# Performance work log

Hardware: AMD Instinct MI355X
Metric: run time of the kernel (lower is better)

The kernel has to match this reference:

```python
import jax, jax.numpy as jnp
import numpy as np

N_HEAD, D_MODEL, D_VOCAB = 8, 512, 32000
B, P = 8, 512


def setup_inputs() -> dict:
    key = jax.random.key(0)
    k_x, k_w, k_b = jax.random.split(key, 3)
    input_tensor = jax.random.normal(k_x, (B, P, N_HEAD, D_MODEL), dtype=jnp.float32)
    # per-head Linear params, torch layout: weight [d_vocab, d_model], bias [d_vocab]
    bound = 1.0 / np.sqrt(D_MODEL)
    weights = jax.random.uniform(k_w, (N_HEAD, D_VOCAB, D_MODEL), minval=-bound, maxval=bound, dtype=jnp.float32)
    biases = jax.random.uniform(k_b, (N_HEAD, D_VOCAB), minval=-bound, maxval=bound, dtype=jnp.float32)
    return {"input_tensor": input_tensor, "weights": weights, "biases": biases}


def reference(input_tensor, weights, biases) -> jnp.ndarray:
    # sum_h (x[:,:,h,:] @ W_h^T + b_h)  -> single contraction over (h, d)
    # input_tensor: [B, P, H, D]; weights: [H, V, D]; biases: [H, V]
    out = jnp.einsum("bphd,hvd->bpv", input_tensor, weights)
    out = out + biases.sum(axis=0)  # [V] broadcast over [B, P, V]
    return out
```

## Files before the change

### kernel.cpp

```cpp
#include <hip/hip_runtime.h>
#include <hip/hip_bf16.h>
#include <stdint.h>

#define NHEAD 8
#define DMODEL 512
#define DVOCAB 32000
#define M_DIM 4096
#define K_DIM 4096
#define N_DIM 32000
#define NT    64

typedef short bf16x8 __attribute__((ext_vector_type(8)));
typedef float f32x4 __attribute__((ext_vector_type(4)));
typedef unsigned short ushort8 __attribute__((ext_vector_type(8)));

template <int V> struct IC { static constexpr int v = V; };

__device__ __forceinline__ unsigned short f2bf(float f) {
    unsigned int u = __builtin_bit_cast(unsigned int, f);
    u = (u + 0x7fffu + ((u >> 16) & 1u)) >> 16;
    return (unsigned short)u;
}

__device__ __forceinline__ void load16_to_lds(const void* g, void* l) {
    __builtin_amdgcn_global_load_lds(
        (const __attribute__((address_space(1))) unsigned int*)g,
        (__attribute__((address_space(3))) unsigned int*)l, 16, 0, 0);
}

__global__ void cvt_x(const float* __restrict__ in, unsigned short* __restrict__ out) {
    long t = (long)blockIdx.x * 256 + threadIdx.x;
    const float4* s = (const float4*)in + t * 2;
    float4 a = s[0], b = s[1];
    ushort8 o;
    o[0] = f2bf(a.x); o[1] = f2bf(a.y); o[2] = f2bf(a.z); o[3] = f2bf(a.w);
    o[4] = f2bf(b.x); o[5] = f2bf(b.y); o[6] = f2bf(b.z); o[7] = f2bf(b.w);
    *(ushort8*)(out + t * 8) = o;
}

__global__ void cvt_w(const float* __restrict__ in, unsigned short* __restrict__ out) {
    int t = blockIdx.x * 256 + threadIdx.x;
    int d8 = t & 63;
    int hv = t >> 6;
    int h = hv / DVOCAB;
    int v = hv - h * DVOCAB;
    const float4* s = (const float4*)(in + (long)hv * DMODEL + d8 * 8);
    float4 a = s[0], b = s[1];
    ushort8 o;
    o[0] = f2bf(a.x); o[1] = f2bf(a.y); o[2] = f2bf(a.z); o[3] = f2bf(a.w);
    o[4] = f2bf(b.x); o[5] = f2bf(b.y); o[6] = f2bf(b.z); o[7] = f2bf(b.w);
    *(ushort8*)(out + (long)v * K_DIM + h * DMODEL + d8 * 8) = o;
}

__global__ void bias_red(const float* __restrict__ b, float* __restrict__ out) {
    int v = blockIdx.x * 256 + threadIdx.x;
    if (v >= DVOCAB) return;
    float s = 0.f;
    #pragma unroll
    for (int h = 0; h < NHEAD; ++h) s += b[h * DVOCAB + v];
    out[v] = s;
}

#define BAR()    __builtin_amdgcn_s_barrier()
#define LGKM0()  asm volatile("s_waitcnt lgkmcnt(0)" ::: "memory")
#define VMCNT6() asm volatile("s_waitcnt vmcnt(6)" ::: "memory")
#define VMCNT0() asm volatile("s_waitcnt vmcnt(0)" ::: "memory")

__global__ __launch_bounds__(512, 2) void gemm256(
    const unsigned short* __restrict__ A,
    const unsigned short* __restrict__ B,
    const float* __restrict__ bias,
    float* __restrict__ C)
{
    __shared__ __attribute__((aligned(16))) unsigned short lds[2][2][2][8192];

    const int tid = threadIdx.x;
    const int bid = blockIdx.x;
    const int wg = (bid & 7) * 250 + (bid >> 3);
    const int mt = wg & 15;
    const int nt = wg >> 4;
    const long m0 = (long)mt * 256;
    const long n0 = (long)nt * 256;

    const int wid = tid >> 6, lane = tid & 63;
    const int wr = wid >> 2, wc = wid & 3;
    const int lr = lane & 15, lk = lane >> 4;
    const int swz = lr & 7;

    const unsigned short* pA[2];
    const unsigned short* pB[2];
    #pragma unroll
    for (int ks = 0; ks < 2; ++ks) {
        const int ch = ((ks << 2) | lk) ^ swz;
        pA[ks] = &lds[0][0][0][0] + (wr * 64 + lr) * 64 + ch * 8;
        pB[ks] = &lds[1][0][0][0] + (wc * 32 + lr) * 64 + ch * 8;
    }
    #define LDA(mi, ks, HALF, CURB) \
        (*(const bf16x8*)(pA[ks] + (mi) * 1024 + (HALF) * 16384 + (CURB) * 8192))
    #define LDB(nj, ks, HALF, CURB) \
        (*(const bf16x8*)(pB[ks] + (nj) * 1024 + (HALF) * 16384 + (CURB) * 8192))

    const char* Ab = (const char*)(A + m0 * K_DIM);
    const char* Bb = (const char*)(B + n0 * K_DIM);
    const int row0 = tid >> 3,         c0 = (tid & 7) ^ (row0 & 7);
    const int row1 = (512 + tid) >> 3, c1 = ((512 + tid) & 7) ^ (row1 & 7);
    unsigned int a00 = (unsigned)(row0 * K_DIM + c0 * 8) * 2u;
    unsigned int a01 = (unsigned)(row1 * K_DIM + c1 * 8) * 2u;
    unsigned int a10 = (unsigned)((128 + row0) * K_DIM + c0 * 8) * 2u;
    unsigned int a11 = (unsigned)((128 + row1) * K_DIM + c1 * 8) * 2u;
    unsigned int b00 = a00, b01 = a01, b10 = a10, b11 = a11;

    #define ST_A0(CURB) do { \
        load16_to_lds(Ab + a00, (char*)&lds[0][0][(CURB)][0] + tid * 16); \
        load16_to_lds(Ab + a01, (char*)&lds[0][0][(CURB)][0] + 8192 + tid * 16); \
        a00 += 128; a01 += 128; } while (0)
    #define ST_A1(CURB) do { \
        load16_to_lds(Ab + a10, (char*)&lds[0][1][(CURB)][0] + tid * 16); \
        load16_to_lds(Ab + a11, (char*)&lds[0][1][(CURB)][0] + 8192 + tid * 16); \
        a10 += 128; a11 += 128; } while (0)
    #define ST_B0(CURB) do { \
        load16_to_lds(Bb + b00, (char*)&lds[1][0][(CURB)][0] + tid * 16); \
        load16_to_lds(Bb + b01, (char*)&lds[1][0][(CURB)][0] + 8192 + tid * 16); \
        b00 += 128; b01 += 128; } while (0)
    #define ST_B1(CURB) do { \
        load16_to_lds(Bb + b10, (char*)&lds[1][1][(CURB)][0] + tid * 16); \
        load16_to_lds(Bb + b11, (char*)&lds[1][1][(CURB)][0] + 8192 + tid * 16); \
        b10 += 128; b11 += 128; } while (0)

    f32x4 acc[8][4];
    #pragma unroll
    for (int i = 0; i < 8; ++i)
        #pragma unroll
        for (int j = 0; j < 4; ++j)
            acc[i][j] = (f32x4){0.f, 0.f, 0.f, 0.f};

    bf16x8 af[4][2], bf0[2][2], bf1[2][2];

    ST_A0(0); ST_B0(0); ST_B1(0); ST_A1(0);
    ST_A0(1); ST_B0(1); ST_B1(1);
    VMCNT6();
    BAR();

    auto body = [&](auto curc, int t) {
        constexpr int CUR = decltype(curc)::v;

        #pragma unroll
        for (int mi = 0; mi < 4; ++mi) {
            af[mi][0] = LDA(mi, 0, 0, CUR);
            af[mi][1] = LDA(mi, 1, 0, CUR);
        }
        #pragma unroll
        for (int nj = 0; nj < 2; ++nj) {
            bf0[nj][0] = LDB(nj, 0, 0, CUR);
            bf0[nj][1] = LDB(nj, 1, 0, CUR);
        }
        if (t + 1 < NT) ST_A1(CUR ^ 1);
        BAR(); LGKM0();
        __builtin_amdgcn_s_setprio(1);
        #pragma unroll
        for (int mi = 0; mi < 4; ++mi)
            #pragma unroll
            for (int nj = 0; nj < 2; ++nj)
                #pragma unroll
                for (int ks = 0; ks < 2; ++ks)
                    acc[mi][nj] = __builtin_amdgcn_mfma_f32_16x16x32_bf16(
                        af[mi][ks], bf0[nj][ks], acc[mi][nj], 0, 0, 0);
        __builtin_amdgcn_s_setprio(0);
        BAR();

        #pragma unroll
        for (int nj = 0; nj < 2; ++nj) {
            bf1[nj][0] = LDB(nj, 0, 1, CUR);
            bf1[nj][1] = LDB(nj, 1, 1, CUR);
        }
        if (t + 2 < NT) ST_A0(CUR);
        BAR(); LGKM0();
        __builtin_amdgcn_s_setprio(1);
        #pragma unroll
        for (int mi = 0; mi < 4; ++mi)
            #pragma unroll
            for (int nj = 0; nj < 2; ++nj)
                #pragma unroll
                for (int ks = 0; ks < 2; ++ks)
                    acc[mi][2 + nj] = __builtin_amdgcn_mfma_f32_16x16x32_bf16(
                        af[mi][ks], bf1[nj][ks], acc[mi][2 + nj], 0, 0, 0);
        __builtin_amdgcn_s_setprio(0);
        BAR();

        #pragma unroll
        for (int mi = 0; mi < 4; ++mi) {
            af[mi][0] = LDA(mi, 0, 1, CUR);
            af[mi][1] = LDA(mi, 1, 1, CUR);
        }
        if (t + 2 < NT) ST_B0(CUR);
        BAR(); LGKM0();
        __builtin_amdgcn_s_setprio(1);
        #pragma unroll
        for (int mi = 0; mi < 4; ++mi)
            #pragma unroll
            for (int nj = 0; nj < 2; ++nj)
                #pragma unroll
                for (int ks = 0; ks < 2; ++ks)
                    acc[4 + mi][nj] = __builtin_amdgcn_mfma_f32_16x16x32_bf16(
                        af[mi][ks], bf0[nj][ks], acc[4 + mi][nj], 0, 0, 0);
        __builtin_amdgcn_s_setprio(0);
        BAR();

        if (t + 2 < NT) ST_B1(CUR);
        if (t < NT - 2) { VMCNT6(); } else { VMCNT0(); }
        BAR();
        __builtin_amdgcn_s_setprio(1);
        #pragma unroll
        for (int mi = 0; mi < 4; ++mi)
            #pragma unroll
            for (int nj = 0; nj < 2; ++nj)
                #pragma unroll
                for (int ks = 0; ks < 2; ++ks)
                    acc[4 + mi][2 + nj] = __builtin_amdgcn_mfma_f32_16x16x32_bf16(
                        af[mi][ks], bf1[nj][ks], acc[4 + mi][2 + nj], 0, 0, 0);
        __builtin_amdgcn_s_setprio(0);
        BAR();
    };

    for (int t = 0; t < NT; t += 2) {
        body(IC<0>{}, t);
        body(IC<1>{}, t + 1);
    }
    #undef LDA
    #undef LDB
    #undef ST_A0
    #undef ST_A1
    #undef ST_B0
    #undef ST_B1

    #pragma unroll
    for (int nj = 0; nj < 4; ++nj) {
        const long col = n0 + (nj >> 1) * 128 + wc * 32 + (nj & 1) * 16 + lr;
        const float bs = bias[col];
        #pragma unroll
        for (int mi = 0; mi < 8; ++mi) {
            const long row = m0 + (mi >> 2) * 128 + wr * 64 + (mi & 3) * 16 + lk * 4;
            #pragma unroll
            for (int r = 0; r < 4; ++r)
                __builtin_nontemporal_store(acc[mi][nj][r] + bs,
                                            &C[(row + r) * (long)N_DIM + col]);
        }
    }
}

__global__ void naive_out(const float* __restrict__ x, const float* __restrict__ w,
                          const float* __restrict__ b, float* __restrict__ out) {
    long idx = (long)blockIdx.x * 256 + threadIdx.x;
    if (idx >= (long)M_DIM * N_DIM) return;
    long m = idx / N_DIM;
    int v = (int)(idx - m * N_DIM);
    float s = 0.f;
    for (int h = 0; h < NHEAD; ++h) {
        const float* xr = x + m * K_DIM + h * DMODEL;
        const float* wr = w + ((long)h * DVOCAB + v) * DMODEL;
        float ps = 0.f;
        for (int d = 0; d < DMODEL; ++d) ps += xr[d] * wr[d];
        s += ps + b[h * DVOCAB + v];
    }
    out[idx] = s;
}

extern "C" void kernel_launch(void* const* d_in, const int* in_sizes, int n_in,
                              void* d_out, int out_size, void* d_ws, size_t ws_size,
                              hipStream_t stream) {
    const float* x = (const float*)d_in[0];
    const float* w = (const float*)d_in[1];
    const float* b = (const float*)d_in[2];
    float* out = (float*)d_out;

    const size_t xbf_bytes = (size_t)M_DIM * K_DIM * 2;
    const size_t wbf_bytes = (size_t)N_DIM * K_DIM * 2;
    const size_t bs_bytes  = (size_t)N_DIM * 4;
    const size_t need = xbf_bytes + wbf_bytes + bs_bytes;

    if (ws_size < need) {
        long total = (long)M_DIM * N_DIM;
        int blocks = (int)((total + 255) / 256);
        naive_out<<<blocks, 256, 0, stream>>>(x, w, b, out);
        return;
    }

    unsigned short* xbf = (unsigned short*)d_ws;
    unsigned short* wbf = (unsigned short*)((char*)d_ws + xbf_bytes);
    float* bsum = (float*)((char*)d_ws + xbf_bytes + wbf_bytes);

    cvt_x<<<8192, 256, 0, stream>>>(x, xbf);
    cvt_w<<<64000, 256, 0, stream>>>(w, wbf);
    bias_red<<<125, 256, 0, stream>>>(b, bsum);
    gemm256<<<2000, 512, 0, stream>>>(xbf, wbf, bsum, out);
}
```

Measured before the change: 1.085 ms.

## Software-pipeline LDS fragment reads across iterations and drop explicit lgkmcnt waits

Restructures the GEMM main loop so LDS fragment reads for the next tile are issued before the last MFMA quadrant of the current tile. A-fragments are double-buffered in registers (afL/afH), and explicit lgkmcnt(0) waits plus one barrier per phase are removed. Global-to-LDS prefetches are regrouped so the full second stage is in flight before the loop starts. The aim is to hide LDS latency behind MFMA work and cut barrier stalls, at the cost of more registers and tighter ordering assumptions on LDS hazards.

```diff
diff --git a/kernel.cpp b/kernel.cpp
--- a/kernel.cpp
+++ b/kernel.cpp
@@ -62,7 +62,7 @@
 }
 
 #define BAR()    __builtin_amdgcn_s_barrier()
-#define LGKM0()  asm volatile("s_waitcnt lgkmcnt(0)" ::: "memory")
+#define VMCNT8() asm volatile("s_waitcnt vmcnt(8)" ::: "memory")
 #define VMCNT6() asm volatile("s_waitcnt vmcnt(6)" ::: "memory")
 #define VMCNT0() asm volatile("s_waitcnt vmcnt(0)" ::: "memory")
 
@@ -127,6 +127,19 @@
         load16_to_lds(Bb + b11, (char*)&lds[1][1][(CURB)][0] + 8192 + tid * 16); \
         b10 += 128; b11 += 128; } while (0)
 
+    #define MFQUAD(AF, BF, MO, NO) do {                                        \
+        _Pragma("unroll")                                                      \
+        for (int ks = 0; ks < 2; ++ks)                                         \
+            _Pragma("unroll")                                                  \
+            for (int mi = 0; mi < 4; ++mi)                                     \
+                _Pragma("unroll")                                              \
+                for (int nj = 0; nj < 2; ++nj)                                 \
+                    acc[(MO) + mi][(NO) + nj] =                                \
+                        __builtin_amdgcn_mfma_f32_16x16x32_bf16(               \
+                            AF[mi][ks], BF[nj][ks], acc[(MO) + mi][(NO) + nj], \
+                            0, 0, 0);                                          \
+    } while (0)
+
     f32x4 acc[8][4];
     #pragma unroll
     for (int i = 0; i < 8; ++i)
@@ -134,92 +147,70 @@
         for (int j = 0; j < 4; ++j)
             acc[i][j] = (f32x4){0.f, 0.f, 0.f, 0.f};
 
-    bf16x8 af[4][2], bf0[2][2], bf1[2][2];
+    bf16x8 afL[4][2], afH[4][2], bf0[2][2], bf1[2][2];
 
     ST_A0(0); ST_B0(0); ST_B1(0); ST_A1(0);
-    ST_A0(1); ST_B0(1); ST_B1(1);
-    VMCNT6();
+    ST_A0(1); ST_B0(1); ST_B1(1); ST_A1(1);
+    VMCNT8();
     BAR();
+    #pragma unroll
+    for (int mi = 0; mi < 4; ++mi) {
+        afL[mi][0] = LDA(mi, 0, 0, 0);
+        afL[mi][1] = LDA(mi, 1, 0, 0);
+    }
+    #pragma unroll
+    for (int nj = 0; nj < 2; ++nj) {
+        bf0[nj][0] = LDB(nj, 0, 0, 0);
+        bf0[nj][1] = LDB(nj, 1, 0, 0);
+    }
 
     auto body = [&](auto curc, int t) {
         constexpr int CUR = decltype(curc)::v;
-
-        #pragma unroll
-        for (int mi = 0; mi < 4; ++mi) {
-            af[mi][0] = LDA(mi, 0, 0, CUR);
-            af[mi][1] = LDA(mi, 1, 0, CUR);
-        }
-        #pragma unroll
-        for (int nj = 0; nj < 2; ++nj) {
-            bf0[nj][0] = LDB(nj, 0, 0, CUR);
-            bf0[nj][1] = LDB(nj, 1, 0, CUR);
-        }
-        if (t + 1 < NT) ST_A1(CUR ^ 1);
-        BAR(); LGKM0();
-        __builtin_amdgcn_s_setprio(1);
-        #pragma unroll
-        for (int mi = 0; mi < 4; ++mi)
-            #pragma unroll
-            for (int nj = 0; nj < 2; ++nj)
-                #pragma unroll
-                for (int ks = 0; ks < 2; ++ks)
-                    acc[mi][nj] = __builtin_amdgcn_mfma_f32_16x16x32_bf16(
-                        af[mi][ks], bf0[nj][ks], acc[mi][nj], 0, 0, 0);
-        __builtin_amdgcn_s_setprio(0);
-        BAR();
 
         #pragma unroll
         for (int nj = 0; nj < 2; ++nj) {
             bf1[nj][0] = LDB(nj, 0, 1, CUR);
             bf1[nj][1] = LDB(nj, 1, 1, CUR);
         }
-        if (t + 2 < NT) ST_A0(CUR);
-        BAR(); LGKM0();
-        __builtin_amdgcn_s_setprio(1);
-        #pragma unroll
-        for (int mi = 0; mi < 4; ++mi)
-            #pragma unroll
-            for (int nj = 0; nj < 2; ++nj)
-                #pragma unroll
-                for (int ks = 0; ks < 2; ++ks)
-                    acc[mi][2 + nj] = __builtin_amdgcn_mfma_f32_16x16x32_bf16(
-                        af[mi][ks], bf1[nj][ks], acc[mi][2 + nj], 0, 0, 0);
+        __builtin_amdgcn_s_setprio(1);
+        MFQUAD(afL, bf0, 0, 0);
         __builtin_amdgcn_s_setprio(0);
         BAR();
 
+        if (t + 2 < NT) { ST_A0(CUR); ST_B0(CUR); }
         #pragma unroll
         for (int mi = 0; mi < 4; ++mi) {
-            af[mi][0] = LDA(mi, 0, 1, CUR);
-            af[mi][1] = LDA(mi, 1, 1, CUR);
-        }
-        if (t + 2 < NT) ST_B0(CUR);
-        BAR(); LGKM0();
-        __builtin_amdgcn_s_setprio(1);
-        #pragma unroll
-        for (int mi = 0; mi < 4; ++mi)
-            #pragma unroll
-            for (int nj = 0; nj < 2; ++nj)
-                #pragma unroll
-                for (int ks = 0; ks < 2; ++ks)
-                    acc[4 + mi][nj] = __builtin_amdgcn_mfma_f32_16x16x32_bf16(
-                        af[mi][ks], bf0[nj][ks], acc[4 + mi][nj], 0, 0, 0);
+            afH[mi][0] = LDA(mi, 0, 1, CUR);
+            afH[mi][1] = LDA(mi, 1, 1, CUR);
+        }
+        __builtin_amdgcn_s_setprio(1);
+        MFQUAD(afL, bf1, 0, 2);
         __builtin_amdgcn_s_setprio(0);
         BAR();
 
         if (t + 2 < NT) ST_B1(CUR);
+        __builtin_amdgcn_s_setprio(1);
+        MFQUAD(afH, bf0, 4, 0);
+        __builtin_amdgcn_s_setprio(0);
         if (t < NT - 2) { VMCNT6(); } else { VMCNT0(); }
         BAR();
-        __builtin_amdgcn_s_setprio(1);
-        #pragma unroll
-        for (int mi = 0; mi < 4; ++mi)
+
+        if (t + 2 < NT) ST_A1(CUR);
+        if (t + 1 < NT) {
             #pragma unroll
-            for (int nj = 0; nj < 2; ++nj)
-                #pragma unroll
-                for (int ks = 0; ks < 2; ++ks)
-                    acc[4 + mi][2 + nj] = __builtin_amdgcn_mfma_f32_16x16x32_bf16(
-                        af[mi][ks], bf1[nj][ks], acc[4 + mi][2 + nj], 0, 0, 0);
-        __builtin_amdgcn_s_setprio(0);
-        BAR();
+            for (int mi = 0; mi < 4; ++mi) {
+                afL[mi][0] = LDA(mi, 0, 0, CUR ^ 1);
+                afL[mi][1] = LDA(mi, 1, 0, CUR ^ 1);
+            }
+            #pragma unroll
+            for (int nj = 0; nj < 2; ++nj) {
+                bf0[nj][0] = LDB(nj, 0, 0, CUR ^ 1);
+                bf0[nj][1] = LDB(nj, 1, 0, CUR ^ 1);
+            }
+        }
+        __builtin_amdgcn_s_setprio(1);
+        MFQUAD(afH, bf1, 4, 2);
+        __builtin_amdgcn_s_setprio(0);
     };
 
     for (int t = 0; t < NT; t += 2) {
@@ -232,6 +223,7 @@
     #undef ST_A1
     #undef ST_B0
     #undef ST_B1
+    #undef MFQUAD
 
     #pragma unroll
     for (int nj = 0; nj < 4; ++nj) {
```

New measurement: 1.183 ms. 9.1% more time.

## Switch GEMM inner loop to 32x32x16 MFMA tiles and remap workgroup order

Applied to the files above, without the earlier changes.

Replaces the 16x16x32 bf16 MFMA fragments with 32x32x16 instructions, changing the LDS read addressing, register fragment layout and the epilogue row mapping to match. Each wave now issues fewer, larger MFMAs per phase and reads fewer LDS fragments per FLOP. The block-to-tile mapping is also changed so each XCD handles two adjacent M tiles across consecutive N tiles, aiming for better L2 reuse of B. The larger fragments raise register pressure per wave and change the LDS bank access pattern under the existing swizzle.

```diff
diff --git a/kernel.cpp b/kernel.cpp
--- a/kernel.cpp
+++ b/kernel.cpp
@@ -11,7 +11,7 @@
 #define NT    64
 
 typedef short bf16x8 __attribute__((ext_vector_type(8)));
-typedef float f32x4 __attribute__((ext_vector_type(4)));
+typedef float f32x16 __attribute__((ext_vector_type(16)));
 typedef unsigned short ushort8 __attribute__((ext_vector_type(8)));
 
 template <int V> struct IC { static constexpr int v = V; };
@@ -76,29 +76,28 @@
 
     const int tid = threadIdx.x;
     const int bid = blockIdx.x;
-    const int wg = (bid & 7) * 250 + (bid >> 3);
-    const int mt = wg & 15;
-    const int nt = wg >> 4;
+    const int xcd = bid & 7, j = bid >> 3;
+    const int mt = xcd * 2 + (j & 1);
+    const int nt = j >> 1;
     const long m0 = (long)mt * 256;
     const long n0 = (long)nt * 256;
 
     const int wid = tid >> 6, lane = tid & 63;
     const int wr = wid >> 2, wc = wid & 3;
-    const int lr = lane & 15, lk = lane >> 4;
-    const int swz = lr & 7;
-
-    const unsigned short* pA[2];
-    const unsigned short* pB[2];
-    #pragma unroll
-    for (int ks = 0; ks < 2; ++ks) {
-        const int ch = ((ks << 2) | lk) ^ swz;
-        pA[ks] = &lds[0][0][0][0] + (wr * 64 + lr) * 64 + ch * 8;
-        pB[ks] = &lds[1][0][0][0] + (wc * 32 + lr) * 64 + ch * 8;
+    const int l31 = lane & 31, lhi = lane >> 5, r7 = lane & 7;
+
+    const unsigned short* pA[4];
+    const unsigned short* pB[4];
+    #pragma unroll
+    for (int ks = 0; ks < 4; ++ks) {
+        const int slot = ((ks << 1) | lhi) ^ r7;
+        pA[ks] = &lds[0][0][0][0] + (wr * 64 + l31) * 64 + slot * 8;
+        pB[ks] = &lds[1][0][0][0] + (wc * 32 + l31) * 64 + slot * 8;
     }
     #define LDA(mi, ks, HALF, CURB) \
-        (*(const bf16x8*)(pA[ks] + (mi) * 1024 + (HALF) * 16384 + (CURB) * 8192))
-    #define LDB(nj, ks, HALF, CURB) \
-        (*(const bf16x8*)(pB[ks] + (nj) * 1024 + (HALF) * 16384 + (CURB) * 8192))
+        (*(const bf16x8*)(pA[ks] + (mi) * 2048 + (HALF) * 16384 + (CURB) * 8192))
+    #define LDB(ks, HALF, CURB) \
+        (*(const bf16x8*)(pB[ks] + (HALF) * 16384 + (CURB) * 8192))
 
     const char* Ab = (const char*)(A + m0 * K_DIM);
     const char* Bb = (const char*)(B + n0 * K_DIM);
@@ -127,14 +126,25 @@
         load16_to_lds(Bb + b11, (char*)&lds[1][1][(CURB)][0] + 8192 + tid * 16); \
         b10 += 128; b11 += 128; } while (0)
 
-    f32x4 acc[8][4];
-    #pragma unroll
-    for (int i = 0; i < 8; ++i)
-        #pragma unroll
-        for (int j = 0; j < 4; ++j)
-            acc[i][j] = (f32x4){0.f, 0.f, 0.f, 0.f};
-
-    bf16x8 af[4][2], bf0[2][2], bf1[2][2];
+    #define MFPH(AF, BF, MO, NO) do {                                          \
+        _Pragma("unroll")                                                      \
+        for (int ks = 0; ks < 4; ++ks)                                         \
+            _Pragma("unroll")                                                  \
+            for (int mi = 0; mi < 2; ++mi)                                     \
+                acc[(MO) + mi][NO] = __builtin_amdgcn_mfma_f32_32x32x16_bf16(  \
+                    AF[mi][ks], BF[ks], acc[(MO) + mi][NO], 0, 0, 0);          \
+    } while (0)
+
+    f32x16 acc[4][2];
+    #pragma unroll
+    for (int i = 0; i < 4; ++i)
+        #pragma unroll
+        for (int jn = 0; jn < 2; ++jn)
+            #pragma unroll
+            for (int r = 0; r < 16; ++r)
+                acc[i][jn][r] = 0.f;
+
+    bf16x8 afL[2][4], afH[2][4], bf0[4], bf1[4];
 
     ST_A0(0); ST_B0(0); ST_B1(0); ST_A1(0);
     ST_A0(1); ST_B0(1); ST_B1(1);
@@ -145,64 +155,39 @@
         constexpr int CUR = decltype(curc)::v;
 
         #pragma unroll
-        for (int mi = 0; mi < 4; ++mi) {
-            af[mi][0] = LDA(mi, 0, 0, CUR);
-            af[mi][1] = LDA(mi, 1, 0, CUR);
-        }
-        #pragma unroll
-        for (int nj = 0; nj < 2; ++nj) {
-            bf0[nj][0] = LDB(nj, 0, 0, CUR);
-            bf0[nj][1] = LDB(nj, 1, 0, CUR);
-        }
+        for (int mi = 0; mi < 2; ++mi)
+            #pragma unroll
+            for (int ks = 0; ks < 4; ++ks)
+                afL[mi][ks] = LDA(mi, ks, 0, CUR);
+        #pragma unroll
+        for (int ks = 0; ks < 4; ++ks)
+            bf0[ks] = LDB(ks, 0, CUR);
         if (t + 1 < NT) ST_A1(CUR ^ 1);
         BAR(); LGKM0();
         __builtin_amdgcn_s_setprio(1);
-        #pragma unroll
-        for (int mi = 0; mi < 4; ++mi)
-            #pragma unroll
-            for (int nj = 0; nj < 2; ++nj)
-                #pragma unroll
-                for (int ks = 0; ks < 2; ++ks)
-                    acc[mi][nj] = __builtin_amdgcn_mfma_f32_16x16x32_bf16(
-                        af[mi][ks], bf0[nj][ks], acc[mi][nj], 0, 0, 0);
-        __builtin_amdgcn_s_setprio(0);
-        BAR();
-
-        #pragma unroll
-        for (int nj = 0; nj < 2; ++nj) {
-            bf1[nj][0] = LDB(nj, 0, 1, CUR);
-            bf1[nj][1] = LDB(nj, 1, 1, CUR);
-        }
+        MFPH(afL, bf0, 0, 0);
+        __builtin_amdgcn_s_setprio(0);
+        BAR();
+
+        #pragma unroll
+        for (int ks = 0; ks < 4; ++ks)
+            bf1[ks] = LDB(ks, 1, CUR);
         if (t + 2 < NT) ST_A0(CUR);
         BAR(); LGKM0();
         __builtin_amdgcn_s_setprio(1);
-        #pragma unroll
-        for (int mi = 0; mi < 4; ++mi)
-            #pragma unroll
-            for (int nj = 0; nj < 2; ++nj)
-                #pragma unroll
-                for (int ks = 0; ks < 2; ++ks)
-                    acc[mi][2 + nj] = __builtin_amdgcn_mfma_f32_16x16x32_bf16(
-                        af[mi][ks], bf1[nj][ks], acc[mi][2 + nj], 0, 0, 0);
-        __builtin_amdgcn_s_setprio(0);
-        BAR();
-
-        #pragma unroll
-        for (int mi = 0; mi < 4; ++mi) {
-            af[mi][0] = LDA(mi, 0, 1, CUR);
-            af[mi][1] = LDA(mi, 1, 1, CUR);
-        }
+        MFPH(afL, bf1, 0, 1);
+        __builtin_amdgcn_s_setprio(0);
+        BAR();
+
+        #pragma unroll
+        for (int mi = 0; mi < 2; ++mi)
+            #pragma unroll
+            for (int ks = 0; ks < 4; ++ks)
+                afH[mi][ks] = LDA(mi, ks, 1, CUR);
         if (t + 2 < NT) ST_B0(CUR);
         BAR(); LGKM0();
         __builtin_amdgcn_s_setprio(1);
-        #pragma unroll
-        for (int mi = 0; mi < 4; ++mi)
-            #pragma unroll
-            for (int nj = 0; nj < 2; ++nj)
-                #pragma unroll
-                for (int ks = 0; ks < 2; ++ks)
-                    acc[4 + mi][nj] = __builtin_amdgcn_mfma_f32_16x16x32_bf16(
-                        af[mi][ks], bf0[nj][ks], acc[4 + mi][nj], 0, 0, 0);
+        MFPH(afH, bf0, 2, 0);
         __builtin_amdgcn_s_setprio(0);
         BAR();
 
@@ -210,14 +195,7 @@
         if (t < NT - 2) { VMCNT6(); } else { VMCNT0(); }
         BAR();
         __builtin_amdgcn_s_setprio(1);
-        #pragma unroll
-        for (int mi = 0; mi < 4; ++mi)
-            #pragma unroll
-            for (int nj = 0; nj < 2; ++nj)
-                #pragma unroll
-                for (int ks = 0; ks < 2; ++ks)
-                    acc[4 + mi][2 + nj] = __builtin_amdgcn_mfma_f32_16x16x32_bf16(
-                        af[mi][ks], bf1[nj][ks], acc[4 + mi][2 + nj], 0, 0, 0);
+        MFPH(afH, bf1, 2, 1);
         __builtin_amdgcn_s_setprio(0);
         BAR();
     };
@@ -232,18 +210,21 @@
     #undef ST_A1
     #undef ST_B0
     #undef ST_B1
-
-    #pragma unroll
-    for (int nj = 0; nj < 4; ++nj) {
-        const long col = n0 + (nj >> 1) * 128 + wc * 32 + (nj & 1) * 16 + lr;
+    #undef MFPH
+
+    #pragma unroll
+    for (int nj = 0; nj < 2; ++nj) {
+        const long col = n0 + nj * 128 + wc * 32 + l31;
         const float bs = bias[col];
         #pragma unroll
-        for (int mi = 0; mi < 8; ++mi) {
-            const long row = m0 + (mi >> 2) * 128 + wr * 64 + (mi & 3) * 16 + lk * 4;
-            #pragma unroll
-            for (int r = 0; r < 4; ++r)
+        for (int mi = 0; mi < 4; ++mi) {
+            const long rowb = m0 + (mi >> 1) * 128 + wr * 64 + (mi & 1) * 32 + lhi * 4;
+            #pragma unroll
+            for (int r = 0; r < 16; ++r) {
+                const long row = rowb + (r & 3) + 8 * (r >> 2);
                 __builtin_nontemporal_store(acc[mi][nj][r] + bs,
-                                            &C[(row + r) * (long)N_DIM + col]);
+                                            &C[row * (long)N_DIM + col]);
+            }
         }
     }
 }
```

After: 1.145 ms. 1.06x slower.
